# Kernel tuning notes

Hardware: AMD Instinct MI355X
Metric: run time of the kernel (lower is better)

## Reference

```python
import jax, jax.numpy as jnp
import numpy as np

MD = 4       # max displacement per level (md=[4,...] in VCN)
WSIZE = 3    # truncation window half-size in flow_reg


def _corrf(ref, tar, md=MD):
    """VCN.corrf: per-channel shifted-product 4D cost volume + leaky_relu.
    cost[b,c,i,j,y,x] = leaky_relu(ref[b,c,y,x] * tar[b,c,y+(j-md), x+(i-md)], 0.1)
    (zero outside valid region, matching the torch zero-filled buffer)."""
    B, C, H, W = ref.shape
    U = 2 * md + 1
    tar_pad = jnp.pad(tar, ((0, 0), (0, 0), (md, md), (md, md)))
    # dim 2 ordered as i*U + j (i = x-shift index, j = y-shift index)
    shifts = jnp.stack([tar_pad[:, :, j:j + H, i:i + W]
                        for i in range(U) for j in range(U)], axis=2)
    cost = jax.nn.leaky_relu(ref[:, :, None] * shifts, 0.1)
    return cost.reshape(B, C, U, U, H, W)


def _flow_reg(x, md=MD, wsize=WSIZE):
    """flow_reg with ent=True: argmax -> 7x7 box mask over (u,v) (the MaxPool3d on a
    one-hot scatter is exactly a Chebyshev-box around the argmax) -> masked softmax
    over u*v -> soft-argmax flow + local/global entropies."""
    B, U, V, H, W = x.shape
    idx = jnp.argmax(x.reshape(B, U * V, H, W), axis=1)         # (B,H,W)
    ub, vb = idx // V, idx % V
    uu = jnp.arange(U)[None, :, None, None, None]
    vv = jnp.arange(V)[None, None, :, None, None]
    mask = (jnp.abs(uu - ub[:, None, None]) <= wsize) & \
           (jnp.abs(vv - vb[:, None, None]) <= wsize)           # (B,U,V,H,W)
    neg_inf = jnp.array(-jnp.inf, x.dtype)
    p = jax.nn.softmax(jnp.where(mask, x, neg_inf).reshape(B, U * V, H, W),
                       axis=1).reshape(B, U, V, H, W)
    fx = (jnp.arange(U) - md).astype(x.dtype)[None, :, None, None, None]
    fy = (jnp.arange(V) - md).astype(x.dtype)[None, None, :, None, None]
    outx = jnp.sum(p * fx, axis=(1, 2))[:, None]                # (B,1,H,W)
    outy = jnp.sum(p * fy, axis=(1, 2))[:, None]
    def _ent(q):
        return (-q * jnp.log(jnp.clip(q, 1e-9, 1 - 1e-9))).sum(axis=(1, 2))[:, None]
    local_ent = _ent(p) / np.log((2 * wsize + 1) ** 2).astype(np.float32)
    pg = jax.nn.softmax(x.reshape(B, U * V, H, W), axis=1).reshape(B, U, V, H, W)
    global_ent = _ent(pg) / np.log(U * V).astype(np.float32)
    return jnp.concatenate([outx, outy], 1), jnp.concatenate([local_ent, global_ent], 1)


def _warp(x, flo):
    """grid_sample-based backward warp (bilinear, zero padding, align_corners=True)
    plus the in-bounds mask, exactly as VCN's warp()."""
    B, C, H, W = x.shape
    px = jnp.arange(W, dtype=flo.dtype)[None, None, :] + flo[:, 0]   # (B,H,W)
    py = jnp.arange(H, dtype=flo.dtype)[None, :, None] + flo[:, 1]
    inb = (jnp.abs(2.0 * px / max(W - 1, 1) - 1.0) < 1) & \
          (jnp.abs(2.0 * py / max(H - 1, 1) - 1.0) < 1)
    x0 = jnp.floor(px); y0 = jnp.floor(py)
    wx = px - x0; wy = py - y0
    x0i = x0.astype(jnp.int32); y0i = y0.astype(jnp.int32)
    flat = x.reshape(B, C, H * W)
    def tap(yi, xi, wgt):
        valid = (xi >= 0) & (xi < W) & (yi >= 0) & (yi < H)
        lin = jnp.clip(yi, 0, H - 1) * W + jnp.clip(xi, 0, W - 1)
        v = jax.vmap(lambda img, l: img[:, l])(flat, lin)            # (B,C,H,W)
        return v * (wgt * valid.astype(x.dtype))[:, None]
    out = (tap(y0i,     x0i,     (1 - wx) * (1 - wy)) +
           tap(y0i,     x0i + 1, wx * (1 - wy)) +
           tap(y0i + 1, x0i,     (1 - wx) * wy) +
           tap(y0i + 1, x0i + 1, wx * wy))
    return out * inb.astype(x.dtype)[:, None], inb


def setup_inputs() -> dict:
    key = jax.random.key(0)
    k1, k2, k3 = jax.random.split(key, 3)
    B, C, H, W, F = 2, 128, 64, 64, 16
    ref = jax.random.normal(k1, (B, C, H, W), jnp.float32) * 0.5
    tar = jax.random.normal(k2, (B, C, H, W), jnp.float32) * 0.5
    pw = jax.random.normal(k3, (F, C), jnp.float32) / np.sqrt(C).astype(np.float32)
    return {"ref_feat": ref, "tar_feat": tar, "proj_w": pw}


def reference(ref_feat, tar_feat, proj_w):
    B, C, H, W = ref_feat.shape
    F_ = proj_w.shape[0]
    U = 2 * MD + 1
    cost = _corrf(ref_feat, tar_feat)                       # (B,C,U,U,H,W)
    # 1x1 channel contraction of the 4D cost volume (butterfly4D input proj)
    cvol = jnp.einsum('bcuvhw,fc->bfuvhw', cost, proj_w)    # (B,F,U,U,H,W)
    flow_h, ent_h = _flow_reg(cvol.reshape(B * F_, U, U, H, W))
    flow = flow_h.reshape(B, F_, 2, H, W)[:, 0]             # first hypothesis
    warped, _ = _warp(tar_feat, flow)
    return jnp.concatenate([flow_h, ent_h], axis=1), warped
```

## Files before the change

### kernel.cpp

```cpp
#include <hip/hip_runtime.h>
#include <math.h>

#define B_ 2
#define C_ 128
#define H_ 64
#define W_ 64
#define F_ 16
#define U_ 9
#define MD_ 4
#define UV_ 81
#define HW_ (H_*W_)
#define BF_ (B_*F_)

typedef float f32x4 __attribute__((ext_vector_type(4)));
typedef float f32x2 __attribute__((ext_vector_type(2)));
typedef _Float16 f16x2 __attribute__((ext_vector_type(2)));
typedef _Float16 f16x4 __attribute__((ext_vector_type(4)));
typedef _Float16 f16x8 __attribute__((ext_vector_type(8)));

#define XSCALE   64.0f
#define WSCALE   256.0f
#define UNSCALE  (1.0f / 16384.0f)

#define TSTR 34
#define REFO 7344
#define SM_  5832
#define SI_  6344
#define SU_  6856
#define LDSZ 9928

static __device__ __forceinline__ f16x8 cat4(f16x2 a, f16x2 b, f16x2 c, f16x2 d) {
    f16x4 ab = __builtin_shufflevector(a, b, 0, 1, 2, 3);
    f16x4 cd = __builtin_shufflevector(c, d, 0, 1, 2, 3);
    return __builtin_shufflevector(ab, cd, 0, 1, 2, 3, 4, 5, 6, 7);
}

static __device__ __forceinline__ void split2(f32x2 p, f16x2& hi, f16x2& lo) {
    hi = __builtin_bit_cast(f16x2, __builtin_amdgcn_cvt_pkrtz(p.x, p.y));
    f32x2 hf; hf.x = (float)hi.x; hf.y = (float)hi.y;
    f32x2 l = p - hf;
    lo = __builtin_bit_cast(f16x2, __builtin_amdgcn_cvt_pkrtz(l.x, l.y));
}

__global__ __launch_bounds__(512, 2)
void fused_kernel(const float* __restrict__ ref,
                  const float* __restrict__ tar,
                  const float* __restrict__ pw,
                  float* __restrict__ out0) {
    const int t    = threadIdx.x;
    const int lane = t & 63;
    const int wid  = t >> 6;
    const int ml   = lane & 15;
    const int grp  = lane >> 4;

    const int n0 = blockIdx.x;
    const int L  = (n0 & 7) * 64 + (n0 >> 3);
    const int b  = L >> 8;
    const int y  = (L >> 2) & 63;
    const int x0 = (L & 3) * 16;

    const int start = wid ? (1 + wid * 10) : 0;

    __shared__ float lds[LDSZ];

    const float* refB = ref + ((size_t)b * C_) * HW_ + y * W_ + x0;
    const float* tarB = tar + ((size_t)b * C_) * HW_;

    int uA[11], vA[11];
    #pragma unroll
    for (int i = 0; i < 11; ++i) {
        int uv = start + i;
        int uu = uv / 9;
        uA[i] = uu; vA[i] = uv - uu * 9;
    }

    #pragma unroll
    for (int it = 0; it < 4; ++it) {
        int idx = it * 512 + t;
        int c = idx >> 4, px = idx & 15;
        lds[REFO + px * 132 + c] = refB[(size_t)c * HW_ + px] * XSCALE;
    }

    float nstg[14];
#define SISSUE(KC) {                                                          \
    _Pragma("unroll")                                                         \
    for (int it = 0; it < 14; ++it) {                                         \
        int idx = it * 512 + t;                                               \
        int c0  = idx / 216;                                                  \
        int rm  = idx - c0 * 216;                                             \
        int r   = rm / 24;                                                    \
        int col = rm - r * 24;                                                \
        int ysr = y + r - 4;                                                  \
        int xg  = x0 - 4 + col;                                               \
        bool ok = (idx < 6912) && ((unsigned)ysr < 64u) && ((unsigned)xg < 64u); \
        int cc  = c0 > 31 ? 31 : c0;                                          \
        int ysc = ysr < 0 ? 0 : (ysr > 63 ? 63 : ysr);                        \
        int xgc = xg  < 0 ? 0 : (xg  > 63 ? 63 : xg);                         \
        float vL = tarB[(size_t)((KC) * 32 + cc) * HW_ + ysc * W_ + xgc];     \
        nstg[it] = ok ? vL : 0.f;                                             \
    } }

#define SWRITE() {                                                            \
    _Pragma("unroll")                                                         \
    for (int it = 0; it < 14; ++it) {                                         \
        int idx = it * 512 + t;                                               \
        if (idx < 6912) {                                                     \
            int c0 = idx / 216;                                               \
            int rm = idx - c0 * 216;                                          \
            lds[rm * TSTR + c0] = nstg[it];                                   \
        }                                                                     \
    } }

    f32x4 acc[11];
    #pragma unroll
    for (int i = 0; i < 11; ++i) acc[i] = f32x4{0.f, 0.f, 0.f, 0.f};

    SISSUE(0);

    for (int kc = 0; kc < 4; ++kc) {
        f32x4 wa = *(const f32x4*)(pw + ml * C_ + kc * 32 + grp * 8);
        f32x4 wb = *(const f32x4*)(pw + ml * C_ + kc * 32 + grp * 8 + 4);

        __syncthreads();
        SWRITE();
        if (kc < 3) SISSUE(kc + 1);
        __syncthreads();

        f16x2 wh[4], wl[4];
        {
            f32x2 p;
            p.x = wa.x * WSCALE; p.y = wa.y * WSCALE; split2(p, wh[0], wl[0]);
            p.x = wa.z * WSCALE; p.y = wa.w * WSCALE; split2(p, wh[1], wl[1]);
            p.x = wb.x * WSCALE; p.y = wb.y * WSCALE; split2(p, wh[2], wl[2]);
            p.x = wb.z * WSCALE; p.y = wb.w * WSCALE; split2(p, wh[3], wl[3]);
        }
        f16x8 whi = cat4(wh[0], wh[1], wh[2], wh[3]);
        f16x8 wlo = cat4(wl[0], wl[1], wl[2], wl[3]);

        f32x4 rva = *(const f32x4*)(lds + REFO + ml * 132 + kc * 32 + grp * 8);
        f32x4 rvb = *(const f32x4*)(lds + REFO + ml * 132 + kc * 32 + grp * 8 + 4);
        f32x2 rv2[4];
        rv2[0].x = rva.x; rv2[0].y = rva.y;
        rv2[1].x = rva.z; rv2[1].y = rva.w;
        rv2[2].x = rvb.x; rv2[2].y = rvb.y;
        rv2[3].x = rvb.z; rv2[3].y = rvb.w;

#define UVBODY(i) {                                                           \
        const int cb = (vA[i] * 24 + ml + uA[i]) * TSTR + grp * 8;            \
        f16x2 xh4[4], xl4[4];                                                 \
        _Pragma("unroll")                                                     \
        for (int jp = 0; jp < 4; ++jp) {                                      \
            f32x2 tj = *(const f32x2*)(lds + cb + 2 * jp);                    \
            f32x2 p  = rv2[jp] * tj;                                          \
            f32x2 p1 = p * 0.1f;                                              \
            p = __builtin_elementwise_max(p, p1);                             \
            split2(p, xh4[jp], xl4[jp]);                                      \
        }                                                                     \
        f16x8 xhi = cat4(xh4[0], xh4[1], xh4[2], xh4[3]);                     \
        f16x8 xlo = cat4(xl4[0], xl4[1], xl4[2], xl4[3]);                     \
        acc[i] = __builtin_amdgcn_mfma_f32_16x16x32_f16(whi, xhi, acc[i], 0, 0, 0); \
        acc[i] = __builtin_amdgcn_mfma_f32_16x16x32_f16(wlo, xhi, acc[i], 0, 0, 0); \
        acc[i] = __builtin_amdgcn_mfma_f32_16x16x32_f16(whi, xlo, acc[i], 0, 0, 0); }

        #pragma unroll
        for (int i = 0; i < 10; ++i) UVBODY(i);
        if (wid == 0) UVBODY(10);
    }
    __syncthreads();

    const int rem = t & 63;
    const int fl  = rem >> 4;
    const int px  = rem & 15;

    for (int P = 0; P < 4; ++P) {
#define BOUNCE(i) {                                                           \
        if (grp == P) {                                                       \
            int ba = (start + (i)) * 18 + ml;                                 \
            lds[ba        ] = acc[i][0] * UNSCALE;                            \
            lds[ba + 1458 ] = acc[i][1] * UNSCALE;                            \
            lds[ba + 2916 ] = acc[i][2] * UNSCALE;                            \
            lds[ba + 4374 ] = acc[i][3] * UNSCALE; } }
        #pragma unroll
        for (int i = 0; i < 10; ++i) BOUNCE(i);
        if (wid == 0) BOUNCE(10);
        __syncthreads();

        float vv[11];
        #pragma unroll
        for (int i = 0; i < 10; ++i)
            vv[i] = lds[fl * 1458 + (start + i) * 18 + px];
        if (wid == 0) vv[10] = lds[fl * 1458 + 10 * 18 + px];
        float mv = vv[0]; int bi = start;
        #pragma unroll
        for (int i = 1; i < 10; ++i)
            if (vv[i] > mv) { mv = vv[i]; bi = start + i; }
        if (wid == 0 && vv[10] > mv) { mv = vv[10]; bi = 10; }
        lds[SM_ + t] = mv; lds[SI_ + t] = (float)bi;
        __syncthreads();

        float m = lds[SM_ + rem]; int best = (int)lds[SI_ + rem];
        #pragma unroll
        for (int k = 1; k < 8; ++k) {
            float mk = lds[SM_ + k * 64 + rem];
            if (mk > m) { m = mk; best = (int)lds[SI_ + k * 64 + rem]; }
        }
        int ub = best / 9, vb = best - 9 * (best / 9);

        float S = 0.f, A = 0.f, Sx = 0.f, Sy = 0.f, gS = 0.f, gA = 0.f;
#define PH2B(i) {                                                             \
        float d = vv[i] - m; float z = __expf(d);                             \
        gS += z; gA = fmaf(z, d, gA);                                         \
        int duc = uA[i] - ub, dvc = vA[i] - vb;                               \
        bool msk = (duc <= 3) && (duc >= -3) && (dvc <= 3) && (dvc >= -3);    \
        float zm = msk ? z : 0.f, dm = msk ? d : 0.f;                         \
        S += zm; A = fmaf(zm, dm, A);                                         \
        Sx = fmaf(zm, (float)(uA[i] - MD_), Sx);                              \
        Sy = fmaf(zm, (float)(vA[i] - MD_), Sy); }
        #pragma unroll
        for (int i = 0; i < 10; ++i) PH2B(i);
        if (wid == 0) PH2B(10);

        lds[SU_ + 0 * 512 + t] = S;  lds[SU_ + 1 * 512 + t] = A;
        lds[SU_ + 2 * 512 + t] = Sx; lds[SU_ + 3 * 512 + t] = Sy;
        lds[SU_ + 4 * 512 + t] = gS; lds[SU_ + 5 * 512 + t] = gA;
        __syncthreads();

        if (t < 64) {
            float rq[6];
            #pragma unroll
            for (int q = 0; q < 6; ++q) {
                float s = lds[SU_ + q * 512 + t];
                #pragma unroll
                for (int k = 1; k < 8; ++k) s += lds[SU_ + q * 512 + k * 64 + t];
                rq[q] = s;
            }
            float invS = 1.f / rq[0];
            float outx = rq[2] * invS;
            float outy = rq[3] * invS;
            float lent = (logf(rq[0]) - rq[1] * invS) * (1.0f / logf(49.0f));
            float gent = (logf(rq[4]) - rq[5] / rq[4]) * (1.0f / logf(81.0f));
            float* op = out0 + ((size_t)(b * F_ + P * 4 + (t >> 4)) * 4) * HW_
                      + y * W_ + x0 + (t & 15);
            op[0 * HW_] = outx;
            op[1 * HW_] = outy;
            op[2 * HW_] = lent;
            op[3 * HW_] = gent;
        }
        __syncthreads();
    }
}

__global__ __launch_bounds__(256)
void warp_kernel(const float* __restrict__ tar,
                 const float* __restrict__ out0,
                 float* __restrict__ warped) {
    int tid = blockIdx.x * 256 + threadIdx.x;
    int pix = tid & (HW_ - 1);
    int bc  = tid >> 12;
    int b   = bc >> 7;
    int x = pix & 63, y = pix >> 6;

    const float* fbase = out0 + (size_t)(b * F_) * 4 * HW_;
    float fx = fbase[pix];
    float fy = fbase[HW_ + pix];
    float px = (float)x + fx;
    float py = (float)y + fy;

    bool inb = (fabsf(2.0f * px / (float)(W_ - 1) - 1.0f) < 1.0f) &&
               (fabsf(2.0f * py / (float)(H_ - 1) - 1.0f) < 1.0f);

    float x0 = floorf(px), y0 = floorf(py);
    float wx = px - x0,    wy = py - y0;
    int x0i = (int)x0, y0i = (int)y0;

    const float* img = tar + (size_t)bc * HW_;

    auto tap = [&](int yi, int xi, float wgt) -> float {
        bool v = ((unsigned)xi < (unsigned)W_) && ((unsigned)yi < (unsigned)H_);
        int xc = xi < 0 ? 0 : (xi > W_ - 1 ? W_ - 1 : xi);
        int yc = yi < 0 ? 0 : (yi > H_ - 1 ? H_ - 1 : yi);
        float val = img[yc * W_ + xc];
        return val * (v ? wgt : 0.f);
    };

    float acc = tap(y0i,     x0i,     (1.f - wx) * (1.f - wy))
              + tap(y0i,     x0i + 1, wx * (1.f - wy))
              + tap(y0i + 1, x0i,     (1.f - wx) * wy)
              + tap(y0i + 1, x0i + 1, wx * wy);

    warped[tid] = inb ? acc : 0.f;
}

extern "C" void kernel_launch(void* const* d_in, const int* in_sizes, int n_in,
                              void* d_out, int out_size, void* d_ws, size_t ws_size,
                              hipStream_t stream) {
    const float* ref = (const float*)d_in[0];
    const float* tar = (const float*)d_in[1];
    const float* pw  = (const float*)d_in[2];
    float* out0 = (float*)d_out;
    float* out1 = out0 + (size_t)BF_ * 4 * HW_;
    (void)d_ws; (void)ws_size;

    fused_kernel<<<512, 512, 0, stream>>>(ref, tar, pw, out0);
    warp_kernel<<<(B_ * C_ * HW_) / 256, 256, 0, stream>>>(tar, out0, out1);
}
```

Measured before the change: 112.6 us.

## Fuse warp into main kernel and double-buffer target staging in LDS

The separate warp kernel is folded into the tail of the fused kernel: after the first hypothesis flow is computed for the block's 16 pixels, it is kept in LDS and used to bilinearly sample all 128 target channels directly. This removes a second launch and the global round trip of the flow. The target-tile staging also changes from register-staged single buffering with two barriers per chunk to direct global-to-LDS double buffering with one barrier per chunk. In exchange, each thread now copies a contiguous channel segment, which can cause LDS bank conflicts and uncoalesced global reads. LDS use per block grows from about 40 KB to about 67 KB, which may limit how many blocks fit on a CU.

```diff
diff --git a/kernel.cpp b/kernel.cpp
--- a/kernel.cpp
+++ b/kernel.cpp
@@ -8,7 +8,6 @@
 #define F_ 16
 #define U_ 9
 #define MD_ 4
-#define UV_ 81
 #define HW_ (H_*W_)
 #define BF_ (B_*F_)
 
@@ -22,12 +21,16 @@
 #define WSCALE   256.0f
 #define UNSCALE  (1.0f / 16384.0f)
 
+#define TB0  0
+#define TB1  7344
 #define TSTR 34
-#define REFO 7344
+#define REFO 14688
 #define SM_  5832
 #define SI_  6344
 #define SU_  6856
-#define LDSZ 9928
+#define FX_  9928
+#define FY_  9944
+#define LDSZ 16800
 
 static __device__ __forceinline__ f16x8 cat4(f16x2 a, f16x2 b, f16x2 c, f16x2 d) {
     f16x4 ab = __builtin_shufflevector(a, b, 0, 1, 2, 3);
@@ -46,7 +49,8 @@
 void fused_kernel(const float* __restrict__ ref,
                   const float* __restrict__ tar,
                   const float* __restrict__ pw,
-                  float* __restrict__ out0) {
+                  float* __restrict__ out0,
+                  float* __restrict__ warped) {
     const int t    = threadIdx.x;
     const int lane = t & 63;
     const int wid  = t >> 6;
@@ -81,51 +85,47 @@
         lds[REFO + px * 132 + c] = refB[(size_t)c * HW_ + px] * XSCALE;
     }
 
-    float nstg[14];
-#define SISSUE(KC) {                                                          \
-    _Pragma("unroll")                                                         \
-    for (int it = 0; it < 14; ++it) {                                         \
-        int idx = it * 512 + t;                                               \
-        int c0  = idx / 216;                                                  \
-        int rm  = idx - c0 * 216;                                             \
-        int r   = rm / 24;                                                    \
-        int col = rm - r * 24;                                                \
-        int ysr = y + r - 4;                                                  \
-        int xg  = x0 - 4 + col;                                               \
-        bool ok = (idx < 6912) && ((unsigned)ysr < 64u) && ((unsigned)xg < 64u); \
-        int cc  = c0 > 31 ? 31 : c0;                                          \
-        int ysc = ysr < 0 ? 0 : (ysr > 63 ? 63 : ysr);                        \
-        int xgc = xg  < 0 ? 0 : (xg  > 63 ? 63 : xg);                         \
-        float vL = tarB[(size_t)((KC) * 32 + cc) * HW_ + ysc * W_ + xgc];     \
-        nstg[it] = ok ? vL : 0.f;                                             \
-    } }
-
-#define SWRITE() {                                                            \
-    _Pragma("unroll")                                                         \
-    for (int it = 0; it < 14; ++it) {                                         \
-        int idx = it * 512 + t;                                               \
-        if (idx < 6912) {                                                     \
-            int c0 = idx / 216;                                               \
-            int rm = idx - c0 * 216;                                          \
-            lds[rm * TSTR + c0] = nstg[it];                                   \
-        }                                                                     \
-    } }
+    const int seg   = t >> 1;
+    const int chalf = (t & 1) * 16;
+    const bool sactive = (seg < 216);
+    const int sr   = seg / 24;
+    const int scol = seg - sr * 24;
+    const int ysr  = y + sr - 4;
+    const int xg   = x0 - 4 + scol;
+    const bool sok = sactive && ((unsigned)ysr < 64u) && ((unsigned)xg < 64u);
+    const int ysc  = ysr < 0 ? 0 : (ysr > 63 ? 63 : ysr);
+    const int xgc  = xg  < 0 ? 0 : (xg  > 63 ? 63 : xg);
+    const float* tS = tarB + (size_t)chalf * HW_ + ysc * W_ + xgc;
+
+    auto STAGE = [&](int kcv, int bufbase, bool zfill) {
+        if (sok) {
+            float* dst = lds + bufbase + seg * TSTR + chalf;
+            const float* g = tS + (size_t)(kcv * 32) * HW_;
+            #pragma unroll
+            for (int c0 = 0; c0 < 16; ++c0) dst[c0] = g[(size_t)c0 * HW_];
+        } else if (sactive && zfill) {
+            float* dst = lds + bufbase + seg * TSTR + chalf;
+            #pragma unroll
+            for (int c0 = 0; c0 < 16; ++c0) dst[c0] = 0.f;
+        }
+    };
 
     f32x4 acc[11];
     #pragma unroll
     for (int i = 0; i < 11; ++i) acc[i] = f32x4{0.f, 0.f, 0.f, 0.f};
 
-    SISSUE(0);
-
+    STAGE(0, TB0, true);
+    __syncthreads();
+
+    #pragma unroll
     for (int kc = 0; kc < 4; ++kc) {
+        const int tb = (kc & 1) ? TB1 : TB0;
+        if (kc == 0) STAGE(1, TB1, true);
+        else if (kc == 1) STAGE(2, TB0, false);
+        else if (kc == 2) STAGE(3, TB1, false);
+
         f32x4 wa = *(const f32x4*)(pw + ml * C_ + kc * 32 + grp * 8);
         f32x4 wb = *(const f32x4*)(pw + ml * C_ + kc * 32 + grp * 8 + 4);
-
-        __syncthreads();
-        SWRITE();
-        if (kc < 3) SISSUE(kc + 1);
-        __syncthreads();
-
         f16x2 wh[4], wl[4];
         {
             f32x2 p;
@@ -146,7 +146,7 @@
         rv2[3].x = rvb.z; rv2[3].y = rvb.w;
 
 #define UVBODY(i) {                                                           \
-        const int cb = (vA[i] * 24 + ml + uA[i]) * TSTR + grp * 8;            \
+        const int cb = tb + (vA[i] * 24 + ml + uA[i]) * TSTR + grp * 8;       \
         f16x2 xh4[4], xl4[4];                                                 \
         _Pragma("unroll")                                                     \
         for (int jp = 0; jp < 4; ++jp) {                                      \
@@ -165,8 +165,9 @@
         #pragma unroll
         for (int i = 0; i < 10; ++i) UVBODY(i);
         if (wid == 0) UVBODY(10);
-    }
-    __syncthreads();
+
+        __syncthreads();
+    }
 
     const int rem = t & 63;
     const int fl  = rem >> 4;
@@ -245,50 +246,42 @@
             op[1 * HW_] = outy;
             op[2 * HW_] = lent;
             op[3 * HW_] = gent;
-        }
-        __syncthreads();
-    }
-}
-
-__global__ __launch_bounds__(256)
-void warp_kernel(const float* __restrict__ tar,
-                 const float* __restrict__ out0,
-                 float* __restrict__ warped) {
-    int tid = blockIdx.x * 256 + threadIdx.x;
-    int pix = tid & (HW_ - 1);
-    int bc  = tid >> 12;
-    int b   = bc >> 7;
-    int x = pix & 63, y = pix >> 6;
-
-    const float* fbase = out0 + (size_t)(b * F_) * 4 * HW_;
-    float fx = fbase[pix];
-    float fy = fbase[HW_ + pix];
-    float px = (float)x + fx;
-    float py = (float)y + fy;
-
-    bool inb = (fabsf(2.0f * px / (float)(W_ - 1) - 1.0f) < 1.0f) &&
-               (fabsf(2.0f * py / (float)(H_ - 1) - 1.0f) < 1.0f);
-
-    float x0 = floorf(px), y0 = floorf(py);
-    float wx = px - x0,    wy = py - y0;
-    int x0i = (int)x0, y0i = (int)y0;
-
-    const float* img = tar + (size_t)bc * HW_;
-
-    auto tap = [&](int yi, int xi, float wgt) -> float {
-        bool v = ((unsigned)xi < (unsigned)W_) && ((unsigned)yi < (unsigned)H_);
-        int xc = xi < 0 ? 0 : (xi > W_ - 1 ? W_ - 1 : xi);
-        int yc = yi < 0 ? 0 : (yi > H_ - 1 ? H_ - 1 : yi);
-        float val = img[yc * W_ + xc];
-        return val * (v ? wgt : 0.f);
-    };
-
-    float acc = tap(y0i,     x0i,     (1.f - wx) * (1.f - wy))
-              + tap(y0i,     x0i + 1, wx * (1.f - wy))
-              + tap(y0i + 1, x0i,     (1.f - wx) * wy)
-              + tap(y0i + 1, x0i + 1, wx * wy);
-
-    warped[tid] = inb ? acc : 0.f;
+            if (P == 0 && t < 16) { lds[FX_ + t] = outx; lds[FY_ + t] = outy; }
+        }
+    }
+
+    {
+        const int pxi = t & 15;
+        const int xw  = x0 + pxi;
+        float fx = lds[FX_ + pxi], fy = lds[FY_ + pxi];
+        float pxw = (float)xw + fx;
+        float pyw = (float)y  + fy;
+        bool inb = (fabsf(2.0f * pxw / 63.0f - 1.0f) < 1.0f) &&
+                   (fabsf(2.0f * pyw / 63.0f - 1.0f) < 1.0f);
+        float xf = floorf(pxw), yf = floorf(pyw);
+        float wx = pxw - xf, wy = pyw - yf;
+        int x0i = (int)xf, y0i = (int)yf;
+        auto off = [&](int yi, int xi, float wgt, float& mw) -> int {
+            bool v = ((unsigned)xi < (unsigned)W_) && ((unsigned)yi < (unsigned)H_);
+            int xc = xi < 0 ? 0 : (xi > W_ - 1 ? W_ - 1 : xi);
+            int yc = yi < 0 ? 0 : (yi > H_ - 1 ? H_ - 1 : yi);
+            mw = v ? wgt : 0.f;
+            return yc * W_ + xc;
+        };
+        float m00, m01, m10, m11;
+        int o00 = off(y0i,     x0i,     (1.f - wx) * (1.f - wy), m00);
+        int o01 = off(y0i,     x0i + 1, wx * (1.f - wy),         m01);
+        int o10 = off(y0i + 1, x0i,     (1.f - wx) * wy,         m10);
+        int o11 = off(y0i + 1, x0i + 1, wx * wy,                 m11);
+        #pragma unroll
+        for (int it = 0; it < 4; ++it) {
+            int c = (t >> 4) + 32 * it;
+            const float* img = tarB + (size_t)c * HW_;
+            float a = img[o00] * m00 + img[o01] * m01
+                    + img[o10] * m10 + img[o11] * m11;
+            warped[((size_t)(b * C_ + c)) * HW_ + y * W_ + xw] = inb ? a : 0.f;
+        }
+    }
 }
 
 extern "C" void kernel_launch(void* const* d_in, const int* in_sizes, int n_in,
@@ -301,6 +294,5 @@
     float* out1 = out0 + (size_t)BF_ * 4 * HW_;
     (void)d_ws; (void)ws_size;
 
-    fused_kernel<<<512, 512, 0, stream>>>(ref, tar, pw, out0);
-    warp_kernel<<<(B_ * C_ * HW_) / 256, 256, 0, stream>>>(tar, out0, out1);
-}
+    fused_kernel<<<512, 512, 0, stream>>>(ref, tar, pw, out0, out1);
+}
```

Measured after the change: 106.6 us. -5.4%, faster.
